# Kernel tuning notes

Hardware: AMD Instinct MI355X
Metric: run time of the kernel (lower is better)

The kernel has to match this reference:

```python
import jax, jax.numpy as jnp
import numpy as np

IN_CH = 128
HID = 256   # 2 * out_channels
OUT_CH = 128
N_NODES = 10000
N_EDGES = 640000


def setup_inputs() -> dict:
    key = jax.random.key(0)
    ks = jax.random.split(key, 6)
    x = jax.random.normal(ks[0], (N_NODES, IN_CH), dtype=jnp.float32)
    edge_index = jax.random.randint(ks[1], (2, N_EDGES), 0, N_NODES, dtype=jnp.int64)
    # GCNConv params (glorot-like scale)
    W1 = jax.random.normal(ks[2], (IN_CH, HID), dtype=jnp.float32) / np.sqrt(IN_CH)
    b1 = jnp.zeros((HID,), dtype=jnp.float32)
    W2 = jax.random.normal(ks[3], (HID, OUT_CH), dtype=jnp.float32) / np.sqrt(HID)
    b2 = jnp.zeros((OUT_CH,), dtype=jnp.float32)
    return {"x": x, "edge_index": edge_index, "W1": W1, "b1": b1, "W2": W2, "b2": b2}


def _gcn_norm(edge_index, n_nodes):
    """Add self-loops and compute symmetric GCN normalization per edge."""
    loops = jnp.arange(n_nodes, dtype=edge_index.dtype)
    src = jnp.concatenate([edge_index[0], loops])  # [E+N]
    dst = jnp.concatenate([edge_index[1], loops])
    deg = jax.ops.segment_sum(jnp.ones_like(dst, dtype=jnp.float32), dst,
                              num_segments=n_nodes)
    dinv = jnp.where(deg > 0, jax.lax.rsqrt(deg), 0.0)
    norm = dinv[src] * dinv[dst]  # [E+N]
    return src, dst, norm


def _gcn_layer(x, W, b, src, dst, norm, n_nodes):
    h = x @ W                                  # [N, F_out]
    msg = h[src] * norm[:, None]               # gather + scale, [E+N, F_out]
    agg = jax.ops.segment_sum(msg, dst, num_segments=n_nodes)
    return agg + b


def reference(x, edge_index, W1, b1, W2, b2):
    n = x.shape[0]
    src, dst, norm = _gcn_norm(edge_index, n)
    h = jax.nn.relu(_gcn_layer(x, W1, b1, src, dst, norm, n))
    out = jax.nn.relu(_gcn_layer(h, W2, b2, src, dst, norm, n))
    return out
```

## Files before the change

kernel.cpp:

```cpp
#include <hip/hip_runtime.h>

#define N_FEAT 128
#define HID 256
#define OUT_CH 128

#define NB 256
#define MAXN 10240

typedef unsigned short u16;
typedef _Float16 f16x8 __attribute__((ext_vector_type(8)));
typedef float f32x4 __attribute__((ext_vector_type(4)));

__device__ __forceinline__ unsigned pack_f16x2(float lo, float hi) {
    union { _Float16 h[2]; unsigned u; } c;
    c.h[0] = (_Float16)lo;
    c.h[1] = (_Float16)hi;
    return c.u;
}
__device__ __forceinline__ float2 unpack_f16x2(unsigned u) {
    union { unsigned u; _Float16 h[2]; } c;
    c.u = u;
    return make_float2((float)c.h[0], (float)c.h[1]);
}
__device__ __forceinline__ u16 f16u(float f) {
    union { _Float16 h; u16 u; } c;
    c.h = (_Float16)f;
    return c.u;
}


__global__ __launch_bounds__(256)
void hist_kernel(const int* __restrict__ dst, u16* __restrict__ bh,
                 int E, int N, int chunk) {
    __shared__ int hist[MAXN];
    for (int i = threadIdx.x; i < N; i += 256) hist[i] = 0;
    __syncthreads();
    int base = blockIdx.x * chunk;
    int lim = min(chunk, E - base);
    for (int i = threadIdx.x; i < lim; i += 256) {
        int d = dst[base + i];
        if (d >= 0 && d < N) atomicAdd(&hist[d], 1);
    }
    __syncthreads();
    u16* out = bh + (size_t)blockIdx.x * N;
    for (int i = threadIdx.x; i < N; i += 256) out[i] = (u16)hist[i];
}

__global__ __launch_bounds__(256)
void colscan_kernel(u16* __restrict__ bh,
                    int* __restrict__ counts, float* __restrict__ dinv, int N) {
    int j = blockIdx.x * 256 + threadIdx.x;
    if (j >= N) return;
    int run = 0;
    #pragma unroll 8
    for (int b = 0; b < NB; b++) {
        size_t idx = (size_t)b * N + j;
        int t = bh[idx];
        bh[idx] = (u16)run;
        run += t;
    }
    counts[j] = run;
    dinv[j] = rsqrtf((float)(run + 1));
}

#define SCAN_T 1024
#define SCAN_MAX_PER 16
__global__ __launch_bounds__(SCAN_T)
void scan_kernel(const int* __restrict__ counts,
                 int* __restrict__ row_start, int n) {
    int tid = threadIdx.x;
    int per = (n + SCAN_T - 1) / SCAN_T;
    int base = tid * per;
    int local[SCAN_MAX_PER];
    int sum = 0;
    for (int j = 0; j < per; j++) {
        int i = base + j;
        int c = (i < n) ? counts[i] : 0;
        local[j] = sum;
        sum += c;
    }
    int lane = tid & 63;
    int wave = tid >> 6;
    int incl = sum;
    #pragma unroll
    for (int off = 1; off < 64; off <<= 1) {
        int t = __shfl_up(incl, off, 64);
        if (lane >= off) incl += t;
    }
    __shared__ int wsum[16];
    __shared__ int woff[16];
    if (lane == 63) wsum[wave] = incl;
    __syncthreads();
    if (wave == 0) {
        int w = (lane < 16) ? wsum[lane] : 0;
        int v = w;
        #pragma unroll
        for (int off = 1; off < 16; off <<= 1) {
            int t = __shfl_up(v, off, 64);
            if (lane >= off) v += t;
        }
        if (lane < 16) woff[lane] = v - w;
    }
    __syncthreads();
    int thread_excl = woff[wave] + (incl - sum);
    for (int j = 0; j < per; j++) {
        int i = base + j;
        if (i < n) row_start[i] = thread_excl + local[j];
    }
    if (tid == SCAN_T - 1) row_start[n] = thread_excl + sum;
}

__global__ __launch_bounds__(256)
void scat_kernel(const int* __restrict__ src, const int* __restrict__ dst,
                 const u16* __restrict__ bh,
                 const int* __restrict__ row_start,
                 int* __restrict__ csr_src, int E, int N, int chunk) {
    __shared__ int cur[MAXN];
    const u16* basep = bh + (size_t)blockIdx.x * N;
    for (int i = threadIdx.x; i < N; i += 256)
        cur[i] = row_start[i] + (int)basep[i];
    __syncthreads();
    int base = blockIdx.x * chunk;
    int lim = min(chunk, E - base);
    for (int i = threadIdx.x; i < lim; i += 256) {
        int e = base + i;
        int d = dst[e];
        if (d < 0 || d >= N) continue;
        int pos = atomicAdd(&cur[d], 1);
        if ((unsigned)pos < (unsigned)E) csr_src[pos] = src[e];
    }
}

__global__ void prescale_kernel(const float* __restrict__ x,
                                const float* __restrict__ dinv,
                                unsigned* __restrict__ xs_b,
                                const float* __restrict__ W1,
                                const float* __restrict__ W2,
                                u16* __restrict__ W1t, u16* __restrict__ W2t,
                                int total4) {
    int i = blockIdx.x * blockDim.x + threadIdx.x;
    if (i < total4) {
        int row = i >> 5;
        float d = dinv[row];
        float4 v = ((const float4*)x)[i];
        uint2 p;
        p.x = pack_f16x2(v.x * d, v.y * d);
        p.y = pack_f16x2(v.z * d, v.w * d);
        ((uint2*)xs_b)[i] = p;
    } else {
        int j = i - total4;
        if (j < N_FEAT * HID) {
            int n = j >> 7, k = j & 127;
            W1t[j] = f16u(W1[(size_t)k * HID + n]);
        } else {
            j -= N_FEAT * HID;
            if (j < HID * OUT_CH) {
                int n = j >> 8, k = j & 255;
                W2t[j] = f16u(W2[(size_t)k * OUT_CH + n]);
            }
        }
    }
}

template <bool EPILOGUE, bool F16OUT>
__global__ __launch_bounds__(256)
void agg_kernel(const unsigned* __restrict__ featb,
                const float* __restrict__ dinv,
                const int* __restrict__ row_start,
                const int* __restrict__ csr_src,
                const float* __restrict__ bias,
                void* __restrict__ out, int N) {
    int wave = threadIdx.x >> 6;
    int n = blockIdx.x * 4 + wave;
    if (n >= N) return;
    int f = threadIdx.x & 63;
    float dn = dinv[n];
    float2 v = unpack_f16x2(featb[(size_t)n * 64 + f]);
    float accx = v.x;
    float accy = v.y;
    int e0 = row_start[n];
    int e1 = row_start[n + 1];
    int e = e0;
    if (e + 8 <= e1) {
        int s_cur[8];
        #pragma unroll
        for (int j = 0; j < 8; j++) s_cur[j] = csr_src[e + j];
        e += 8;
        for (; e + 8 <= e1; e += 8) {
            unsigned w[8];
            #pragma unroll
            for (int j = 0; j < 8; j++) w[j] = featb[(size_t)s_cur[j] * 64 + f];
            int s_nxt[8];
            #pragma unroll
            for (int j = 0; j < 8; j++) s_nxt[j] = csr_src[e + j];
            #pragma unroll
            for (int j = 0; j < 8; j++) {
                float2 u = unpack_f16x2(w[j]);
                accx += u.x;
                accy += u.y;
            }
            #pragma unroll
            for (int j = 0; j < 8; j++) s_cur[j] = s_nxt[j];
        }
        unsigned w[8];
        #pragma unroll
        for (int j = 0; j < 8; j++) w[j] = featb[(size_t)s_cur[j] * 64 + f];
        #pragma unroll
        for (int j = 0; j < 8; j++) {
            float2 u = unpack_f16x2(w[j]);
            accx += u.x;
            accy += u.y;
        }
    }
    for (; e + 4 <= e1; e += 4) {
        int s0 = csr_src[e], s1 = csr_src[e + 1];
        int s2 = csr_src[e + 2], s3 = csr_src[e + 3];
        unsigned w0 = featb[(size_t)s0 * 64 + f];
        unsigned w1 = featb[(size_t)s1 * 64 + f];
        unsigned w2 = featb[(size_t)s2 * 64 + f];
        unsigned w3 = featb[(size_t)s3 * 64 + f];
        float2 u0 = unpack_f16x2(w0), u1 = unpack_f16x2(w1);
        float2 u2 = unpack_f16x2(w2), u3 = unpack_f16x2(w3);
        accx += u0.x + u1.x + u2.x + u3.x;
        accy += u0.y + u1.y + u2.y + u3.y;
    }
    for (; e < e1; ++e) {
        float2 u = unpack_f16x2(featb[(size_t)csr_src[e] * 64 + f]);
        accx += u.x;
        accy += u.y;
    }
    accx *= dn;
    accy *= dn;
    if (EPILOGUE) {
        float2 b = ((const float2*)bias)[f];
        accx = fmaxf(accx + b.x, 0.0f);
        accy = fmaxf(accy + b.y, 0.0f);
    }
    if (F16OUT) {
        ((unsigned*)out)[(size_t)n * 64 + f] = pack_f16x2(accx, accy);
    } else {
        float2 r;
        r.x = accx;
        r.y = accy;
        ((float2*)out)[(size_t)n * 64 + f] = r;
    }
}

template <bool BIAS_RELU, bool RSCALE>
__global__ __launch_bounds__(256)
void gemm16_kernel(const u16* __restrict__ A,
                   const u16* __restrict__ Bt,
                   const float* __restrict__ bias,
                   const float* __restrict__ rscale,
                   u16* __restrict__ C,
                   int M, int N, int K) {
    __shared__ __align__(16) u16 As[64][64];
    __shared__ __align__(16) u16 Bs[64][64];
    int tid = threadIdx.x;
    int w = tid >> 6;
    int l = tid & 63;
    int m0 = blockIdx.y * 64;
    int n0 = blockIdx.x * 64;

    f32x4 acc[4];
    const f32x4 zero = {0.f, 0.f, 0.f, 0.f};
    #pragma unroll
    for (int n = 0; n < 4; n++) acc[n] = zero;

    int rowA = w * 16 + (l & 15);
    int cbase = l >> 4;

    for (int k0 = 0; k0 < K; k0 += 64) {
        #pragma unroll
        for (int t = 0; t < 2; t++) {
            int q = tid + t * 256;
            int r = q >> 3;
            int c = q & 7;
            f16x8 av = *(const f16x8*)(A + (size_t)(m0 + r) * K + k0 + c * 8);
            *(f16x8*)&As[r][(c ^ (r & 7)) * 8] = av;
            f16x8 bv = *(const f16x8*)(Bt + (size_t)(n0 + r) * K + k0 + c * 8);
            *(f16x8*)&Bs[r][(c ^ (r & 7)) * 8] = bv;
        }
        __syncthreads();
        #pragma unroll
        for (int kc = 0; kc < 2; kc++) {
            int ch = kc * 4 + cbase;
            f16x8 af = *(const f16x8*)&As[rowA][(ch ^ (rowA & 7)) * 8];
            #pragma unroll
            for (int n = 0; n < 4; n++) {
                int rb = n * 16 + (l & 15);
                f16x8 bf = *(const f16x8*)&Bs[rb][(ch ^ (rb & 7)) * 8];
                acc[n] = __builtin_amdgcn_mfma_f32_16x16x32_f16(af, bf, acc[n], 0, 0, 0);
            }
        }
        __syncthreads();
    }
    int r0 = (l >> 4) * 2 * 2;
    int col_l = l & 15;
    #pragma unroll
    for (int r = 0; r < 4; r++) {
        int m = m0 + w * 16 + r0 + r;
        if (m >= M) continue;
        float rs = RSCALE ? rscale[m] : 1.0f;
        #pragma unroll
        for (int n = 0; n < 4; n++) {
            int col = n0 + n * 16 + col_l;
            float v = acc[n][r];
            if (RSCALE) v *= rs;
            if (BIAS_RELU) v = fmaxf(v + bias[col], 0.0f);
            C[(size_t)m * N + col] = f16u(v);
        }
    }
}


static inline size_t align512(size_t x) { return (x + 511) & ~(size_t)511; }

extern "C" void kernel_launch(void* const* d_in, const int* in_sizes, int n_in,
                              void* d_out, int out_size, void* d_ws, size_t ws_size,
                              hipStream_t stream) {
    const float* x = (const float*)d_in[0];
    const int* ei = (const int*)d_in[1];
    const float* W1 = (const float*)d_in[2];
    const float* b1 = (const float*)d_in[3];
    const float* W2 = (const float*)d_in[4];
    const float* b2 = (const float*)d_in[5];
    float* out = (float*)d_out;

    const int N = in_sizes[0] / N_FEAT;
    const int E = in_sizes[1] / 2;
    const int* src = ei;
    const int* dst = ei + E;

    const int Mpad = ((N + 63) / 64) * 64;

    char* ws = (char*)d_ws;
    size_t off = 0;
    float* dinv = (float*)(ws + off);    off += align512((size_t)N * 4);
    int* counts = (int*)(ws + off);      off += align512((size_t)N * 4);
    int* row_start = (int*)(ws + off);   off += align512((size_t)(N + 1) * 4);
    int* csr_src = (int*)(ws + off);     off += align512((size_t)E * 4);
    unsigned* xs_b = (unsigned*)(ws + off);  off += align512((size_t)N * 64 * 4);
    u16* agg1h = (u16*)(ws + off);       off += align512((size_t)Mpad * N_FEAT * 2);
    u16* h16 = (u16*)(ws + off);         off += align512((size_t)Mpad * HID * 2);
    u16* t16 = (u16*)(ws + off);         off += align512((size_t)N * OUT_CH * 2);
    u16* W1t = (u16*)(ws + off);         off += align512((size_t)HID * N_FEAT * 2);
    u16* W2t = (u16*)(ws + off);         off += align512((size_t)OUT_CH * HID * 2);
    u16* bh = (u16*)(ws + off);          off += align512((size_t)NB * N * 2);
    (void)ws_size;
    const int chunk = (E + NB - 1) / NB;
    const int NJ = (N + 255) / 256;

    hist_kernel<<<NB, 256, 0, stream>>>(dst, bh, E, N, chunk);
    colscan_kernel<<<NJ, 256, 0, stream>>>(bh, counts, dinv, N);
    scan_kernel<<<1, SCAN_T, 0, stream>>>(counts, row_start, N);
    scat_kernel<<<NB, 256, 0, stream>>>(src, dst, bh, row_start, csr_src, E, N, chunk);

    {
        int total4 = N * N_FEAT / 4;
        int total = total4 + N_FEAT * HID + HID * OUT_CH;
        prescale_kernel<<<(total + 255) / 256, 256, 0, stream>>>(
            x, dinv, xs_b, W1, W2, W1t, W2t, total4);
    }

    agg_kernel<false, true><<<(N + 3) / 4, 256, 0, stream>>>(
        xs_b, dinv, row_start, csr_src, nullptr, agg1h, N);

    {
        dim3 grid(HID / 64, Mpad / 64);
        gemm16_kernel<true, false><<<grid, 256, 0, stream>>>(
            agg1h, W1t, b1, nullptr, h16, N, HID, N_FEAT);
    }

    {
        dim3 grid(OUT_CH / 64, Mpad / 64);
        gemm16_kernel<false, true><<<grid, 256, 0, stream>>>(
            h16, W2t, nullptr, dinv, t16, N, OUT_CH, HID);
    }

    agg_kernel<true, false><<<(N + 3) / 4, 256, 0, stream>>>(
        (const unsigned*)t16, dinv, row_start, csr_src, b2, out, N);
}
```

Baseline: 179.7 us.

## Fuse CSR build and prescale into one cooperative kernel with grid syncs

Replaces the histogram, column-scan, single-block scan, scatter and prescale kernels with one cooperative kernel of 256 blocks separated by grid.sync barriers. The global prefix scan becomes a two-level scan: 40 blocks scan their columns, then a per-block segment-sum fixup. Idle blocks do the weight transposes and the feature prescaling concurrently. This removes four kernel launches and the serial single-block scan, at the cost of grid-wide barriers and a hardcoded NJ=40 that assumes N <= 10240.

```diff
diff --git a/kernel.cpp b/kernel.cpp
--- a/kernel.cpp
+++ b/kernel.cpp
@@ -1,10 +1,14 @@
 #include <hip/hip_runtime.h>
+#include <hip/hip_cooperative_groups.h>
+
+namespace cg = cooperative_groups;
 
 #define N_FEAT 128
 #define HID 256
 #define OUT_CH 128
 
 #define NB 256
+#define NJ 40
 #define MAXN 10240
 
 typedef unsigned short u16;
@@ -28,136 +32,135 @@
     return c.u;
 }
 
-
 __global__ __launch_bounds__(256)
-void hist_kernel(const int* __restrict__ dst, u16* __restrict__ bh,
-                 int E, int N, int chunk) {
-    __shared__ int hist[MAXN];
-    for (int i = threadIdx.x; i < N; i += 256) hist[i] = 0;
+void csr_coop(const int* __restrict__ dst, const int* __restrict__ src,
+              u16* __restrict__ bh, int* __restrict__ csr_src,
+              int* __restrict__ row_start, int* __restrict__ segsum,
+              float* __restrict__ dinv,
+              const float* __restrict__ x, unsigned* __restrict__ xs_b,
+              const float* __restrict__ W1, const float* __restrict__ W2,
+              u16* __restrict__ W1t, u16* __restrict__ W2t,
+              int E, int N, int chunk) {
+    cg::grid_group grid = cg::this_grid();
+    __shared__ int smem[MAXN];
+    const int tid = threadIdx.x;
+    const int bid = blockIdx.x;
+
+    for (int i = tid; i < N; i += 256) smem[i] = 0;
     __syncthreads();
-    int base = blockIdx.x * chunk;
-    int lim = min(chunk, E - base);
-    for (int i = threadIdx.x; i < lim; i += 256) {
-        int d = dst[base + i];
-        if (d >= 0 && d < N) atomicAdd(&hist[d], 1);
+    {
+        int base = bid * chunk;
+        int lim = min(chunk, E - base);
+        for (int i = tid; i < lim; i += 256) {
+            int d = dst[base + i];
+            if (d >= 0 && d < N) atomicAdd(&smem[d], 1);
+        }
     }
     __syncthreads();
-    u16* out = bh + (size_t)blockIdx.x * N;
-    for (int i = threadIdx.x; i < N; i += 256) out[i] = (u16)hist[i];
-}
-
-__global__ __launch_bounds__(256)
-void colscan_kernel(u16* __restrict__ bh,
-                    int* __restrict__ counts, float* __restrict__ dinv, int N) {
-    int j = blockIdx.x * 256 + threadIdx.x;
-    if (j >= N) return;
-    int run = 0;
-    #pragma unroll 8
-    for (int b = 0; b < NB; b++) {
-        size_t idx = (size_t)b * N + j;
-        int t = bh[idx];
-        bh[idx] = (u16)run;
-        run += t;
-    }
-    counts[j] = run;
-    dinv[j] = rsqrtf((float)(run + 1));
-}
-
-#define SCAN_T 1024
-#define SCAN_MAX_PER 16
-__global__ __launch_bounds__(SCAN_T)
-void scan_kernel(const int* __restrict__ counts,
-                 int* __restrict__ row_start, int n) {
-    int tid = threadIdx.x;
-    int per = (n + SCAN_T - 1) / SCAN_T;
-    int base = tid * per;
-    int local[SCAN_MAX_PER];
-    int sum = 0;
-    for (int j = 0; j < per; j++) {
-        int i = base + j;
-        int c = (i < n) ? counts[i] : 0;
-        local[j] = sum;
-        sum += c;
-    }
-    int lane = tid & 63;
-    int wave = tid >> 6;
-    int incl = sum;
-    #pragma unroll
-    for (int off = 1; off < 64; off <<= 1) {
-        int t = __shfl_up(incl, off, 64);
-        if (lane >= off) incl += t;
-    }
-    __shared__ int wsum[16];
-    __shared__ int woff[16];
-    if (lane == 63) wsum[wave] = incl;
-    __syncthreads();
-    if (wave == 0) {
-        int w = (lane < 16) ? wsum[lane] : 0;
-        int v = w;
-        #pragma unroll
-        for (int off = 1; off < 16; off <<= 1) {
-            int t = __shfl_up(v, off, 64);
-            if (lane >= off) v += t;
-        }
-        if (lane < 16) woff[lane] = v - w;
-    }
-    __syncthreads();
-    int thread_excl = woff[wave] + (incl - sum);
-    for (int j = 0; j < per; j++) {
-        int i = base + j;
-        if (i < n) row_start[i] = thread_excl + local[j];
-    }
-    if (tid == SCAN_T - 1) row_start[n] = thread_excl + sum;
-}
-
-__global__ __launch_bounds__(256)
-void scat_kernel(const int* __restrict__ src, const int* __restrict__ dst,
-                 const u16* __restrict__ bh,
-                 const int* __restrict__ row_start,
-                 int* __restrict__ csr_src, int E, int N, int chunk) {
-    __shared__ int cur[MAXN];
-    const u16* basep = bh + (size_t)blockIdx.x * N;
-    for (int i = threadIdx.x; i < N; i += 256)
-        cur[i] = row_start[i] + (int)basep[i];
-    __syncthreads();
-    int base = blockIdx.x * chunk;
-    int lim = min(chunk, E - base);
-    for (int i = threadIdx.x; i < lim; i += 256) {
-        int e = base + i;
-        int d = dst[e];
-        if (d < 0 || d >= N) continue;
-        int pos = atomicAdd(&cur[d], 1);
-        if ((unsigned)pos < (unsigned)E) csr_src[pos] = src[e];
-    }
-}
-
-__global__ void prescale_kernel(const float* __restrict__ x,
-                                const float* __restrict__ dinv,
-                                unsigned* __restrict__ xs_b,
-                                const float* __restrict__ W1,
-                                const float* __restrict__ W2,
-                                u16* __restrict__ W1t, u16* __restrict__ W2t,
-                                int total4) {
-    int i = blockIdx.x * blockDim.x + threadIdx.x;
-    if (i < total4) {
-        int row = i >> 5;
-        float d = dinv[row];
-        float4 v = ((const float4*)x)[i];
-        uint2 p;
-        p.x = pack_f16x2(v.x * d, v.y * d);
-        p.y = pack_f16x2(v.z * d, v.w * d);
-        ((uint2*)xs_b)[i] = p;
+    {
+        u16* outp = bh + (size_t)bid * N;
+        for (int i = tid; i < N; i += 256) outp[i] = (u16)smem[i];
+    }
+
+    grid.sync();
+
+    int run = 0, local_excl = 0;
+    if (bid < NJ) {
+        int j = bid * 256 + tid;
+        if (j < N) {
+            #pragma unroll 8
+            for (int b = 0; b < NB; b++) {
+                size_t idx = (size_t)b * N + j;
+                int t = bh[idx];
+                bh[idx] = (u16)run;
+                run += t;
+            }
+            dinv[j] = rsqrtf((float)(run + 1));
+        }
+        int lane = tid & 63, wv = tid >> 6;
+        int incl = run;
+        #pragma unroll
+        for (int off = 1; off < 64; off <<= 1) {
+            int t = __shfl_up(incl, off, 64);
+            if (lane >= off) incl += t;
+        }
+        if (lane == 63) smem[wv] = incl;
+        __syncthreads();
+        int wbase = 0;
+        #pragma unroll
+        for (int k = 0; k < 4; k++)
+            if (k < wv) wbase += smem[k];
+        local_excl = wbase + (incl - run);
+        if (tid == 255) segsum[bid] = wbase + incl;
     } else {
-        int j = i - total4;
-        if (j < N_FEAT * HID) {
-            int n = j >> 7, k = j & 127;
-            W1t[j] = f16u(W1[(size_t)k * HID + n]);
-        } else {
-            j -= N_FEAT * HID;
-            if (j < HID * OUT_CH) {
-                int n = j >> 8, k = j & 255;
-                W2t[j] = f16u(W2[(size_t)k * OUT_CH + n]);
-            }
+        int t = (bid - NJ) * 256 + tid;
+        const int stride = (256 - NJ) * 256;
+        const int TOT = N_FEAT * HID + HID * OUT_CH;
+        for (; t < TOT; t += stride) {
+            if (t < N_FEAT * HID) {
+                int n = t >> 7, k = t & 127;
+                W1t[t] = f16u(W1[(size_t)k * HID + n]);
+            } else {
+                int j2 = t - N_FEAT * HID;
+                int n = j2 >> 8, k = j2 & 255;
+                W2t[j2] = f16u(W2[(size_t)k * OUT_CH + n]);
+            }
+        }
+    }
+
+    grid.sync();
+
+    if (bid < NJ) {
+        if (tid < 64) {
+            int v = (tid < NJ) ? segsum[tid] : 0;
+            int incl = v;
+            #pragma unroll
+            for (int off = 1; off < 64; off <<= 1) {
+                int t = __shfl_up(incl, off, 64);
+                if (tid >= off) incl += t;
+            }
+            int excl = incl - v;
+            int base = __shfl(excl, bid, 64);
+            int total = __shfl(incl, NJ - 1, 64);
+            if (tid == 0) {
+                smem[64] = base;
+                if (bid == 0) row_start[N] = total;
+            }
+        }
+        __syncthreads();
+        int base = smem[64];
+        int j = bid * 256 + tid;
+        if (j < N) row_start[j] = base + local_excl;
+    } else {
+        const int total4 = N * N_FEAT / 4;
+        int i = (bid - NJ) * 256 + tid;
+        const int stride = (256 - NJ) * 256;
+        for (; i < total4; i += stride) {
+            int row = i >> 5;
+            float d = dinv[row];
+            float4 v = ((const float4*)x)[i];
+            uint2 p;
+            p.x = pack_f16x2(v.x * d, v.y * d);
+            p.y = pack_f16x2(v.z * d, v.w * d);
+            ((uint2*)xs_b)[i] = p;
+        }
+    }
+
+    grid.sync();
+
+    {
+        const u16* basep = bh + (size_t)bid * N;
+        for (int i = tid; i < N; i += 256)
+            smem[i] = row_start[i] + (int)basep[i];
+        __syncthreads();
+        int base = bid * chunk;
+        int lim = min(chunk, E - base);
+        for (int i = tid; i < lim; i += 256) {
+            int e = base + i;
+            int d = dst[e];
+            if (d < 0 || d >= N) continue;
+            int pos = atomicAdd(&smem[d], 1);
+            if ((unsigned)pos < (unsigned)E) csr_src[pos] = src[e];
         }
     }
 }
@@ -295,7 +298,7 @@
         }
         __syncthreads();
     }
-    int r0 = (l >> 4) * 2 * 2;
+    int r0 = (l >> 4) * 4;
     int col_l = l & 15;
     #pragma unroll
     for (int r = 0; r < 4; r++) {
@@ -337,7 +340,7 @@
     char* ws = (char*)d_ws;
     size_t off = 0;
     float* dinv = (float*)(ws + off);    off += align512((size_t)N * 4);
-    int* counts = (int*)(ws + off);      off += align512((size_t)N * 4);
+    int* segsum = (int*)(ws + off);      off += align512((size_t)64 * 4);
     int* row_start = (int*)(ws + off);   off += align512((size_t)(N + 1) * 4);
     int* csr_src = (int*)(ws + off);     off += align512((size_t)E * 4);
     unsigned* xs_b = (unsigned*)(ws + off);  off += align512((size_t)N * 64 * 4);
@@ -348,19 +351,20 @@
     u16* W2t = (u16*)(ws + off);         off += align512((size_t)OUT_CH * HID * 2);
     u16* bh = (u16*)(ws + off);          off += align512((size_t)NB * N * 2);
     (void)ws_size;
-    const int chunk = (E + NB - 1) / NB;
-    const int NJ = (N + 255) / 256;
-
-    hist_kernel<<<NB, 256, 0, stream>>>(dst, bh, E, N, chunk);
-    colscan_kernel<<<NJ, 256, 0, stream>>>(bh, counts, dinv, N);
-    scan_kernel<<<1, SCAN_T, 0, stream>>>(counts, row_start, N);
-    scat_kernel<<<NB, 256, 0, stream>>>(src, dst, bh, row_start, csr_src, E, N, chunk);
-
-    {
-        int total4 = N * N_FEAT / 4;
-        int total = total4 + N_FEAT * HID + HID * OUT_CH;
-        prescale_kernel<<<(total + 255) / 256, 256, 0, stream>>>(
-            x, dinv, xs_b, W1, W2, W1t, W2t, total4);
+    int chunk = (E + NB - 1) / NB;
+    int Ev = E, Nv = N;
+
+    {
+        const int* dstp = dst;
+        const int* srcp = src;
+        void* kargs[] = {
+            (void*)&dstp, (void*)&srcp, (void*)&bh, (void*)&csr_src,
+            (void*)&row_start, (void*)&segsum, (void*)&dinv,
+            (void*)&x, (void*)&xs_b, (void*)&W1, (void*)&W2,
+            (void*)&W1t, (void*)&W2t, (void*)&Ev, (void*)&Nv, (void*)&chunk
+        };
+        hipLaunchCooperativeKernel(reinterpret_cast<void*>(csr_coop),
+                                   dim3(NB), dim3(256), kargs, 0, stream);
     }
 
     agg_kernel<false, true><<<(N + 3) / 4, 256, 0, stream>>>(
```

New measurement: 271.9 us. +51.4%, slower.
